# Kernel tuning notes

Measured on AMD Instinct MI355X. Metric: run time of the kernel, lower is better.

The kernel has to match this reference:

```python
import jax, jax.numpy as jnp
import numpy as np

N_HEADS = 8      # tree has 8 head indices: 0..7
CHILDREN = 64    # each head has 64 consecutive child indices
N = N_HEADS + N_HEADS * CHILDREN  # 520 total classes
B = 65536        # batch


def _segments():
    # segment 0 = the heads group (tree.keys()); segment i+1 = children of head i
    seg = np.zeros(N, dtype=np.int32)
    for i in range(N_HEADS):
        seg[N_HEADS + i * CHILDREN: N_HEADS + (i + 1) * CHILDREN] = i + 1
    return jnp.asarray(seg)


def setup_inputs() -> dict:
    key = jax.random.key(0)
    x = jax.random.normal(key, (B, N), dtype=jnp.float32)
    return {"x": x, "seg": _segments()}


def reference(x, seg):
    # Fused segmented softmax over columns: each column belongs to exactly one
    # group (heads group or one children group), so the sequential per-group
    # softmax loop in the original is equivalent to one segmented softmax.
    num_seg = N_HEADS + 1
    xT = x.T  # [N, B] -- segment ops reduce over the leading axis
    m = jax.ops.segment_max(xT, seg, num_segments=num_seg)   # [S, B] per-group max
    e = jnp.exp(xT - m[seg])                                  # stable exp
    s = jax.ops.segment_sum(e, seg, num_segments=num_seg)    # [S, B] per-group sum
    return (e / s[seg]).T                                     # [B, N]
```

## Files before the change

### kernel.cpp

```cpp
#include <hip/hip_runtime.h>


#define HS_B 65536
#define HS_N 520
#define HS_NP (HS_B / 2)

typedef float f32x4 __attribute__((ext_vector_type(4)));

__device__ __forceinline__ f32x4 ld_f4(const float* p) {
    return *reinterpret_cast<const f32x4*>(p);
}

__device__ __forceinline__ f32x4 seg_softmax(f32x4 v) {
    f32x4 e;
    e.x = __expf(v.x);
    e.y = __expf(v.y);
    e.z = __expf(v.z);
    e.w = __expf(v.w);
    float s = (e.x + e.y) + (e.z + e.w);
#pragma unroll
    for (int mask = 8; mask >= 1; mask >>= 1)
        s += __shfl_xor(s, mask, 16);
    const float inv = 1.0f / s;
    e.x *= inv; e.y *= inv; e.z *= inv; e.w *= inv;
    return e;
}

__global__ void HierarchicalSoftmax_88914412962167_kernel(
    const float* __restrict__ x, float* __restrict__ out) {
    const int gtid   = blockIdx.x * blockDim.x + threadIdx.x;
    const int wave   = gtid >> 6;
    const int lane   = threadIdx.x & 63;
    const int nwaves = (gridDim.x * blockDim.x) >> 6;

    int pair = wave;
    if (pair >= HS_NP) return;

    const float* x0 = x + (size_t)pair * (2 * HS_N);
    f32x4 v00 = ld_f4(x0 + 8 +        lane * 4);
    f32x4 v01 = ld_f4(x0 + 8 + 256 +  lane * 4);
    f32x4 v10 = ld_f4(x0 + HS_N + 8 +       lane * 4);
    f32x4 v11 = ld_f4(x0 + HS_N + 8 + 256 + lane * 4);
    float h = (lane < 16) ? ((lane < 8) ? x0[lane] : x0[HS_N + lane - 8]) : 0.0f;

    while (true) {
        const int next = pair + nwaves;
        const bool have_next = next < HS_NP;

        const f32x4 e00 = seg_softmax(v00);
        const f32x4 e01 = seg_softmax(v01);
        const f32x4 e10 = seg_softmax(v10);
        const f32x4 e11 = seg_softmax(v11);

        const float eh = __expf(h);
        float sh = eh;
#pragma unroll
        for (int mask = 4; mask >= 1; mask >>= 1)
            sh += __shfl_xor(sh, mask, 8);
        const float oh = eh / sh;

        f32x4 n00, n01, n10, n11;
        float nh = 0.0f;
        if (have_next) {
            const float* xn = x + (size_t)next * (2 * HS_N);
            n00 = ld_f4(xn + 8 +        lane * 4);
            n01 = ld_f4(xn + 8 + 256 +  lane * 4);
            n10 = ld_f4(xn + HS_N + 8 +       lane * 4);
            n11 = ld_f4(xn + HS_N + 8 + 256 + lane * 4);
            nh = (lane < 16) ? ((lane < 8) ? xn[lane] : xn[HS_N + lane - 8]) : 0.0f;
        }

        float* o0 = out + (size_t)pair * (2 * HS_N);
        *reinterpret_cast<f32x4*>(o0 + 8 +        lane * 4) = e00;
        *reinterpret_cast<f32x4*>(o0 + 8 + 256 +  lane * 4) = e01;
        *reinterpret_cast<f32x4*>(o0 + HS_N + 8 +       lane * 4) = e10;
        *reinterpret_cast<f32x4*>(o0 + HS_N + 8 + 256 + lane * 4) = e11;
        if (lane < 16) {
            float* hp = (lane < 8) ? (o0 + lane) : (o0 + HS_N + lane - 8);
            *hp = oh;
        }

        if (!have_next) break;
        v00 = n00; v01 = n01; v10 = n10; v11 = n11; h = nh;
        pair = next;
    }
}

extern "C" void kernel_launch(void* const* d_in, const int* in_sizes, int n_in,
                              void* d_out, int out_size, void* d_ws, size_t ws_size,
                              hipStream_t stream) {
    const float* x = (const float*)d_in[0];
    float* out = (float*)d_out;

    const int block = 256;
    const int grid  = 2048;
    HierarchicalSoftmax_88914412962167_kernel<<<grid, block, 0, stream>>>(x, out);
}
```

Before: 48.53 us.

## Stage row pairs through LDS for fully coalesced global loads and stores

Each wave now loads its pair of rows as contiguous float4 chunks into a per-wave LDS buffer, computes the segmented softmax from LDS, writes the results back to LDS, and then stores them to global memory as contiguous aligned chunks. This replaces the old scattered scalar head-column accesses and the 8-float-offset float4 accesses with aligned contiguous transfers. In exchange it drops the software prefetch of the next pair, adds LDS round trips and two block-wide __syncthreads per iteration, and sets launch bounds. The barriers are block-wide even though each wave uses only its own LDS slice, so waves in a block are serialized against each other.

```diff
diff --git a/kernel.cpp b/kernel.cpp
--- a/kernel.cpp
+++ b/kernel.cpp
@@ -1,13 +1,15 @@
 #include <hip/hip_runtime.h>
 
 
-#define HS_B 65536
-#define HS_N 520
-#define HS_NP (HS_B / 2)
+#define HS_B   65536
+#define HS_N   520
+#define HS_NP  (HS_B / 2)
+#define PAIR_F 1040
+#define LDS_STRIDE 1044
 
 typedef float f32x4 __attribute__((ext_vector_type(4)));
 
-__device__ __forceinline__ f32x4 ld_f4(const float* p) {
+__device__ __forceinline__ f32x4 ldg4(const float* p) {
     return *reinterpret_cast<const f32x4*>(p);
 }
 
@@ -26,32 +28,43 @@
     return e;
 }
 
-__global__ void HierarchicalSoftmax_88914412962167_kernel(
+__global__ __launch_bounds__(256, 8) void HierarchicalSoftmax_88914412962167_kernel(
     const float* __restrict__ x, float* __restrict__ out) {
+    __shared__ float lds[4 * LDS_STRIDE];
     const int gtid   = blockIdx.x * blockDim.x + threadIdx.x;
     const int wave   = gtid >> 6;
     const int lane   = threadIdx.x & 63;
+    const int wid    = threadIdx.x >> 6;
     const int nwaves = (gridDim.x * blockDim.x) >> 6;
+    float* L = lds + wid * LDS_STRIDE;
 
-    int pair = wave;
-    if (pair >= HS_NP) return;
+    for (int pair = wave; pair < HS_NP; pair += nwaves) {
+        const float* g = x + (size_t)pair * PAIR_F;
 
-    const float* x0 = x + (size_t)pair * (2 * HS_N);
-    f32x4 v00 = ld_f4(x0 + 8 +        lane * 4);
-    f32x4 v01 = ld_f4(x0 + 8 + 256 +  lane * 4);
-    f32x4 v10 = ld_f4(x0 + HS_N + 8 +       lane * 4);
-    f32x4 v11 = ld_f4(x0 + HS_N + 8 + 256 + lane * 4);
-    float h = (lane < 16) ? ((lane < 8) ? x0[lane] : x0[HS_N + lane - 8]) : 0.0f;
+        const f32x4 r0 = ldg4(g +        lane * 4);
+        const f32x4 r1 = ldg4(g + 256  + lane * 4);
+        const f32x4 r2 = ldg4(g + 512  + lane * 4);
+        const f32x4 r3 = ldg4(g + 768  + lane * 4);
+        f32x4 r4;
+        if (lane < 4) r4 = ldg4(g + 1024 + lane * 4);
+        *reinterpret_cast<f32x4*>(L +        lane * 4) = r0;
+        *reinterpret_cast<f32x4*>(L + 256  + lane * 4) = r1;
+        *reinterpret_cast<f32x4*>(L + 512  + lane * 4) = r2;
+        *reinterpret_cast<f32x4*>(L + 768  + lane * 4) = r3;
+        if (lane < 4) *reinterpret_cast<f32x4*>(L + 1024 + lane * 4) = r4;
 
-    while (true) {
-        const int next = pair + nwaves;
-        const bool have_next = next < HS_NP;
+        __syncthreads();
+
+        const f32x4 v00 = *reinterpret_cast<const f32x4*>(L + 8   + lane * 4);
+        const f32x4 v01 = *reinterpret_cast<const f32x4*>(L + 264 + lane * 4);
+        const f32x4 v10 = *reinterpret_cast<const f32x4*>(L + 528 + lane * 4);
+        const f32x4 v11 = *reinterpret_cast<const f32x4*>(L + 784 + lane * 4);
+        const float h = (lane < 16) ? ((lane < 8) ? L[lane] : L[520 + lane - 8]) : 0.0f;
 
         const f32x4 e00 = seg_softmax(v00);
         const f32x4 e01 = seg_softmax(v01);
         const f32x4 e10 = seg_softmax(v10);
         const f32x4 e11 = seg_softmax(v11);
-
         const float eh = __expf(h);
         float sh = eh;
 #pragma unroll
@@ -59,30 +72,27 @@
             sh += __shfl_xor(sh, mask, 8);
         const float oh = eh / sh;
 
-        f32x4 n00, n01, n10, n11;
-        float nh = 0.0f;
-        if (have_next) {
-            const float* xn = x + (size_t)next * (2 * HS_N);
-            n00 = ld_f4(xn + 8 +        lane * 4);
-            n01 = ld_f4(xn + 8 + 256 +  lane * 4);
-            n10 = ld_f4(xn + HS_N + 8 +       lane * 4);
-            n11 = ld_f4(xn + HS_N + 8 + 256 + lane * 4);
-            nh = (lane < 16) ? ((lane < 8) ? xn[lane] : xn[HS_N + lane - 8]) : 0.0f;
+        *reinterpret_cast<f32x4*>(L + 8   + lane * 4) = e00;
+        *reinterpret_cast<f32x4*>(L + 264 + lane * 4) = e01;
+        *reinterpret_cast<f32x4*>(L + 528 + lane * 4) = e10;
+        *reinterpret_cast<f32x4*>(L + 784 + lane * 4) = e11;
+        if (lane < 16) L[(lane < 8) ? lane : (520 + lane - 8)] = oh;
+
+        __syncthreads();
+
+        float* o = out + (size_t)pair * PAIR_F;
+        const f32x4 w0 = *reinterpret_cast<const f32x4*>(L +        lane * 4);
+        const f32x4 w1 = *reinterpret_cast<const f32x4*>(L + 256  + lane * 4);
+        const f32x4 w2 = *reinterpret_cast<const f32x4*>(L + 512  + lane * 4);
+        const f32x4 w3 = *reinterpret_cast<const f32x4*>(L + 768  + lane * 4);
+        *reinterpret_cast<f32x4*>(o +        lane * 4) = w0;
+        *reinterpret_cast<f32x4*>(o + 256  + lane * 4) = w1;
+        *reinterpret_cast<f32x4*>(o + 512  + lane * 4) = w2;
+        *reinterpret_cast<f32x4*>(o + 768  + lane * 4) = w3;
+        if (lane < 4) {
+            const f32x4 w4 = *reinterpret_cast<const f32x4*>(L + 1024 + lane * 4);
+            *reinterpret_cast<f32x4*>(o + 1024 + lane * 4) = w4;
         }
-
-        float* o0 = out + (size_t)pair * (2 * HS_N);
-        *reinterpret_cast<f32x4*>(o0 + 8 +        lane * 4) = e00;
-        *reinterpret_cast<f32x4*>(o0 + 8 + 256 +  lane * 4) = e01;
-        *reinterpret_cast<f32x4*>(o0 + HS_N + 8 +       lane * 4) = e10;
-        *reinterpret_cast<f32x4*>(o0 + HS_N + 8 + 256 + lane * 4) = e11;
-        if (lane < 16) {
-            float* hp = (lane < 8) ? (o0 + lane) : (o0 + HS_N + lane - 8);
-            *hp = oh;
-        }
-
-        if (!have_next) break;
-        v00 = n00; v01 = n01; v10 = n10; v11 = n11; h = nh;
-        pair = next;
     }
 }
 
```

Measured after the change: 48.84 us. About the same (+0.6%).
